# Kernel tuning notes

Hardware: AMD Instinct MI355X
Metric: run time of the kernel (lower is better)

The kernel has to match this reference:

```python
import jax, jax.numpy as jnp
import numpy as np

HEAD = 2

def setup_inputs() -> dict:
    key = jax.random.key(0)
    ks = jax.random.split(key, 12)
    B, C, H, W = 4, 512, 64, 64
    IC = 256
    N = H * W
    s = 0.02
    return {
        "x": jax.random.normal(ks[0], (B, C, H, W), jnp.float32),
        "output_attn": jax.random.normal(ks[1], (B, C, H, W), jnp.float32),
        "mlp_w": jax.random.normal(ks[2], (N, N), jnp.float32) * s,
        "mlp_b": jax.random.normal(ks[3], (N,), jnp.float32) * s,
        "g_w": jax.random.normal(ks[4], (IC, C), jnp.float32) * s,
        "g_b": jax.random.normal(ks[5], (IC,), jnp.float32) * s,
        "theta_w": jax.random.normal(ks[6], (IC, C), jnp.float32) * s,
        "theta_b": jax.random.normal(ks[7], (IC,), jnp.float32) * s,
        "phi_w": jax.random.normal(ks[8], (IC, C), jnp.float32) * s,
        "phi_b": jax.random.normal(ks[9], (IC,), jnp.float32) * s,
        "out_w": jax.random.normal(ks[10], (C, IC), jnp.float32) * s,
        "out_b": jax.random.normal(ks[11], (C,), jnp.float32) * s,
    }

def _conv1x1(feat, w, b):
    # feat: [B, Cin, N], w: [Cout, Cin], b: [Cout] -> [B, Cout, N]
    return jnp.einsum('bcn,oc->bon', feat, w) + b[None, :, None]

def reference(x, output_attn, mlp_w, mlp_b, g_w, g_b, theta_w, theta_b,
              phi_w, phi_b, out_w, out_b):
    B, C, H, W = x.shape
    N = H * W
    IC = g_w.shape[0]
    d = IC // HEAD  # per-head dim

    xf = x.reshape(B, C, N)
    # head-MLP remix: only hd==HEAD slice is non-empty (integer-division bug in source)
    xf = xf + (jnp.einsum('bcn,mn->bcm', xf, mlp_w) + mlp_b)

    g = _conv1x1(xf, g_w, g_b)                       # [B, IC, N]
    g = g.reshape(B * HEAD, d, N).transpose(0, 2, 1)  # [BH, N, d]

    oa = output_attn.reshape(B, C, N)
    th = _conv1x1(oa, theta_w, theta_b).reshape(B * HEAD, d, N).transpose(0, 2, 1)  # [BH, N, d]
    ph = _conv1x1(xf, phi_w, phi_b).reshape(B * HEAD, d, N)                          # [BH, d, N]

    scale = 1.0 / (d ** 0.5)
    attn = jax.nn.softmax(jnp.einsum('bnd,bdm->bnm', th, ph) * scale, axis=-1)  # [BH, N, N]
    y = jnp.einsum('bnm,bmd->bnd', attn, g)           # [BH, N, d]
    y = y.reshape(B, HEAD, N, d).transpose(0, 2, 1, 3).reshape(B, N, IC)
    y = y.transpose(0, 2, 1)                          # [B, IC, N]

    out = output_attn + _conv1x1(y, out_w, out_b).reshape(B, C, H, W)
    return out
```

## Files before the change

### kernel.cpp

```cpp
#include <hip/hip_runtime.h>

typedef unsigned short us;
typedef us s8v __attribute__((ext_vector_type(8)));
typedef us s4v __attribute__((ext_vector_type(4)));
typedef float f4v __attribute__((ext_vector_type(4)));
typedef float f16v __attribute__((ext_vector_type(16)));
typedef __bf16 b2v __attribute__((ext_vector_type(2)));

static __device__ __forceinline__ us f2b(float f) {
  return __builtin_bit_cast(us, (__bf16)f);
}
static __device__ __forceinline__ unsigned f2b2(float lo, float hi) {
  b2v v = {(__bf16)lo, (__bf16)hi};
  return __builtin_bit_cast(unsigned, v);
}
static __device__ __forceinline__ float b2f(us s) {
  unsigned u = ((unsigned)s) << 16;
  return __builtin_bit_cast(float, u);
}

#define GLDS(src, dst)                                                        \
  __builtin_amdgcn_global_load_lds(                                           \
      (const __attribute__((address_space(1))) unsigned int*)(src),           \
      (__attribute__((address_space(3))) unsigned int*)(dst), 16, 0, 0)

__global__ __launch_bounds__(256) void castk(const float* __restrict__ in,
                                             us* __restrict__ out, int n4) {
  int i = blockIdx.x * 256 + threadIdx.x;
  int stride = gridDim.x * 256;
  for (; i < n4; i += stride) {
    float4 v = ((const float4*)in)[i];
    s4v s = {f2b(v.x), f2b(v.y), f2b(v.z), f2b(v.w)};
    ((s4v*)out)[i] = s;
  }
}

__global__ __launch_bounds__(256) void wcast4(const float* __restrict__ s0, us* __restrict__ o0,
                                              const float* __restrict__ s1, us* __restrict__ o1,
                                              const float* __restrict__ s2, us* __restrict__ o2,
                                              const float* __restrict__ s3, us* __restrict__ o3) {
  const float* s; us* o;
  int y = blockIdx.y;
  if (y == 0) { s = s0; o = o0; }
  else if (y == 1) { s = s1; o = o1; }
  else if (y == 2) { s = s2; o = o2; }
  else { s = s3; o = o3; }
  int i = blockIdx.x * 256 + threadIdx.x;
  for (; i < 32768; i += 8192) {
    float4 v = ((const float4*)s)[i];
    s4v r = {f2b(v.x), f2b(v.y), f2b(v.z), f2b(v.w)};
    ((s4v*)o)[i] = r;
  }
}

__global__ __launch_bounds__(256) void tcast(const float* __restrict__ in,
                                             us* __restrict__ out, int R, int C) {
  __shared__ float t[64][65];
  const int tid = threadIdx.x;
  const long r0 = (long)blockIdx.y * 64, c0 = (long)blockIdx.x * 64;
#pragma unroll
  for (int j = 0; j < 4; ++j) {
    int idx = j * 256 + tid;
    int row = idx >> 4, c4 = (idx & 15) * 4;
    float4 v = *(const float4*)(in + (r0 + row) * C + c0 + c4);
    t[row][c4] = v.x; t[row][c4 + 1] = v.y; t[row][c4 + 2] = v.z; t[row][c4 + 3] = v.w;
  }
  __syncthreads();
#pragma unroll
  for (int j = 0; j < 4; ++j) {
    int idx = j * 256 + tid;
    int orow = idx >> 4, r4 = (idx & 15) * 4;
    s4v s = {f2b(t[r4][orow]), f2b(t[r4 + 1][orow]), f2b(t[r4 + 2][orow]), f2b(t[r4 + 3][orow])};
    *(s4v*)(out + (c0 + orow) * R + r0 + r4) = s;
  }
}

#define SW(row, kb) ((row) * 128 + ((kb) ^ (((row) & 7) << 4)))

template <int EPI, int AF32, int BF32, int SWZ>
__global__ __launch_bounds__(256) void gemm_nt(
    const void* __restrict__ Av, const void* __restrict__ Bv,
    int lda, int ldb, int K, long aZ, long bZ,
    const float* __restrict__ bias,
    const us* __restrict__ addb16,
    const float* __restrict__ addf32,
    us* __restrict__ outb16,
    float* __restrict__ outf32) {
  __shared__ __align__(16) us lA[128 * 64];
  __shared__ __align__(16) us lB[128 * 64];
  const int tid = threadIdx.x, l = tid & 63;
  const int lr = l & 15, lg = l >> 4;
  const int w = tid >> 6, wr = w >> 1, wc = w & 1;
  int bm, bn;
  if constexpr (SWZ) {
    int flat = blockIdx.y * gridDim.x + blockIdx.x;
    int re = (flat & 7) * ((gridDim.x * gridDim.y) >> 3) + (flat >> 3);
    bm = re % gridDim.x; bn = re / gridDim.x;
  } else { bm = blockIdx.x; bn = blockIdx.y; }
  const int z = blockIdx.z;
  const f4v zero = {0.f, 0.f, 0.f, 0.f};
  f4v acc[4][4];
#pragma unroll
  for (int i = 0; i < 4; ++i)
#pragma unroll
    for (int j = 0; j < 4; ++j) acc[i][j] = zero;
  char* lab = (char*)lA;
  char* lbb = (char*)lB;

  for (int k0 = 0; k0 < K; k0 += 64) {
#pragma unroll
    for (int j = 0; j < 4; ++j) {
      int byte = j * 4096 + tid * 16;
      int row = byte >> 7, kb = byte & 127;
      if constexpr (AF32) {
        const float* af = (const float*)Av + (long)z * aZ + (long)(bm * 128 + row) * lda + k0 + (kb >> 1);
        float4 v0 = *(const float4*)af, v1 = *(const float4*)(af + 4);
        s8v va = {f2b(v0.x), f2b(v0.y), f2b(v0.z), f2b(v0.w), f2b(v1.x), f2b(v1.y), f2b(v1.z), f2b(v1.w)};
        *(s8v*)(lab + SW(row, kb)) = va;
      } else {
        s8v va = *(const s8v*)((const char*)Av + ((long)z * aZ + (long)(bm * 128 + row) * lda + k0) * 2 + kb);
        *(s8v*)(lab + SW(row, kb)) = va;
      }
      if constexpr (BF32) {
        const float* bf_ = (const float*)Bv + (long)z * bZ + (long)(bn * 128 + row) * ldb + k0 + (kb >> 1);
        float4 v0 = *(const float4*)bf_, v1 = *(const float4*)(bf_ + 4);
        s8v vb = {f2b(v0.x), f2b(v0.y), f2b(v0.z), f2b(v0.w), f2b(v1.x), f2b(v1.y), f2b(v1.z), f2b(v1.w)};
        *(s8v*)(lbb + SW(row, kb)) = vb;
      } else {
        s8v vb = *(const s8v*)((const char*)Bv + ((long)z * bZ + (long)(bn * 128 + row) * ldb + k0) * 2 + kb);
        *(s8v*)(lbb + SW(row, kb)) = vb;
      }
    }
    __syncthreads();
#pragma unroll
    for (int ks = 0; ks < 2; ++ks) {
      s8v af[4], bf[4];
      const int kb = ks * 64 + lg * 16;
#pragma unroll
      for (int mi = 0; mi < 4; ++mi) {
        int row = wr * 64 + mi * 16 + lr;
        af[mi] = *(const s8v*)(lab + SW(row, kb));
      }
#pragma unroll
      for (int ni = 0; ni < 4; ++ni) {
        int row = wc * 64 + ni * 16 + lr;
        bf[ni] = *(const s8v*)(lbb + SW(row, kb));
      }
#pragma unroll
      for (int mi = 0; mi < 4; ++mi)
#pragma unroll
        for (int ni = 0; ni < 4; ++ni)
          acc[mi][ni] = __builtin_amdgcn_mfma_f32_16x16x32_bf16(af[mi], bf[ni], acc[mi][ni], 0, 0, 0);
    }
    __syncthreads();
  }

#pragma unroll
  for (int mi = 0; mi < 4; ++mi) {
#pragma unroll
    for (int ni = 0; ni < 4; ++ni) {
#pragma unroll
      for (int r = 0; r < 4; ++r) {
        int row = bm * 128 + wr * 64 + mi * 16 + lg * 4 + r;
        int col = bn * 128 + wc * 64 + ni * 16 + lr;
        float v = acc[mi][ni][r];
        if constexpr (EPI == 0) {
          long idx = (long)row * 2048 + col;
          outb16[idx] = f2b(v + b2f(addb16[idx]) + bias[row]);
        } else if constexpr (EPI == 1) {
          long idx = ((long)(z * 2 + (col >> 7)) * 4096 + row) * 128 + (col & 127);
          outb16[idx] = f2b(v + bias[col]);
        } else if constexpr (EPI == 2) {
          long idx = ((long)(z * 256 + row)) * 4096 + col;
          outb16[idx] = f2b(v + bias[row]);
        } else {
          long idx = ((long)(z * 512 + row)) * 4096 + col;
          outf32[idx] = v + bias[row] + addf32[idx];
        }
      }
    }
  }
}

__global__ __launch_bounds__(256, 2) void attn_k(const us* __restrict__ th,
                                                 const us* __restrict__ pht,
                                                 const us* __restrict__ g,
                                                 us* __restrict__ pY,
                                                 float2* __restrict__ pml) {
  __shared__ __align__(16) us ph2[2][64 * 128];
  __shared__ __align__(16) us g2[2][128 * 64];
  const int tid = threadIdx.x, l = tid & 63, w = tid >> 6;
  const int l31 = l & 31, h = l >> 5;
  const int swz = (l & 7) << 4;
  const int flat = blockIdx.y * 32 + blockIdx.x;
  const int bh = flat & 7, rest = flat >> 3;
  const int half = rest & 1, qb = rest >> 1;
  const int b = bh >> 1, head = bh & 1;
  const int m00 = half * 2048;
  const float C1 = 0.12751802f;
  const f16v zero16 = {0.f};

  const char* phsrc = (const char*)(pht + (long)bh * 4096 * 128);
  const char* gsrc = (const char*)(g + (long)(b * 256 + head * 128) * 4096);

  int koff[4], voff[4];
#pragma unroll
  for (int j = 0; j < 4; ++j) {
    int d = j * 4096 + tid * 16;
    koff[j] = d ^ (((d >> 8) & 7) << 4);
    int rowg = d >> 7, kbg = d & 127;
    voff[j] = rowg * 8192 + (kbg ^ ((rowg & 7) << 4));
  }

  s8v qf[8];
  {
    const us* thp = th + ((long)bh * 4096 + qb * 128 + w * 32 + l31) * 128 + h * 8;
#pragma unroll
    for (int ks = 0; ks < 8; ++ks) qf[ks] = *(const s8v*)(thp + ks * 16);
  }

  f16v acc0 = zero16, acc1 = zero16, acc2 = zero16, acc3 = zero16;
  float m_run = -1e30f, l_run = 0.f;

  auto stage = [&](int bufi, int m0) {
    char* dk = (char*)ph2[bufi] + w * 1024;
    char* dv = (char*)g2[bufi] + w * 1024;
    const char* sk = phsrc + (long)m0 * 256;
    const char* sv = gsrc + (long)m0 * 2;
#pragma unroll
    for (int j = 0; j < 4; ++j) {
      GLDS(sk + koff[j], dk + j * 4096);
      GLDS(sv + voff[j], dv + j * 4096);
    }
  };

  stage(0, m00);
  __syncthreads();

  for (int t = 0; t < 32; ++t) {
    const int cur = t & 1;
    stage(cur ^ 1, m00 + ((t + 1) & 31) * 64);
    const char* phb = (const char*)ph2[cur];
    const char* gb = (const char*)g2[cur];

    f16v sA[2] = {zero16, zero16};
    __builtin_amdgcn_s_setprio(1);
#pragma unroll
    for (int ks = 0; ks < 8; ++ks) {
      const int kb = (ks * 32) ^ swz;
#pragma unroll
      for (int mt = 0; mt < 2; ++mt) {
        s8v kf = *(const s8v*)(phb + (mt * 32 + l31) * 256 + (((ks * 32) + h * 16) ^ swz));
        sA[mt] = __builtin_amdgcn_mfma_f32_32x32x16_bf16(kf, qf[ks], sA[mt], 0, 0, 0);
      }
      (void)kb;
    }
    __builtin_amdgcn_s_setprio(0);

    float mx = sA[0][0];
#pragma unroll
    for (int r = 1; r < 16; ++r) mx = fmaxf(mx, sA[0][r]);
#pragma unroll
    for (int r = 0; r < 16; ++r) mx = fmaxf(mx, sA[1][r]);
    mx = fmaxf(mx, __shfl_xor(mx, 32, 64));

    if (__any(mx > m_run + 60.0f)) {
      float mn = fmaxf(m_run, mx);
      float corr = __builtin_amdgcn_exp2f((m_run - mn) * C1);
      m_run = mn;
      l_run *= corr;
#pragma unroll
      for (int r = 0; r < 16; ++r) {
        acc0[r] *= corr; acc1[r] *= corr; acc2[r] *= corr; acc3[r] *= corr;
      }
    }

    const float nm = -m_run * C1;
    float sum = 0.f;
    s8v bfrag[4];
#pragma unroll
    for (int mt = 0; mt < 2; ++mt) {
#pragma unroll
      for (int k1 = 0; k1 < 2; ++k1) {
        const int base = k1 * 8;
        float p0 = __builtin_amdgcn_exp2f(__builtin_fmaf(sA[mt][base + 0], C1, nm));
        float p1 = __builtin_amdgcn_exp2f(__builtin_fmaf(sA[mt][base + 1], C1, nm));
        float p2 = __builtin_amdgcn_exp2f(__builtin_fmaf(sA[mt][base + 2], C1, nm));
        float p3 = __builtin_amdgcn_exp2f(__builtin_fmaf(sA[mt][base + 3], C1, nm));
        float p4 = __builtin_amdgcn_exp2f(__builtin_fmaf(sA[mt][base + 4], C1, nm));
        float p5 = __builtin_amdgcn_exp2f(__builtin_fmaf(sA[mt][base + 5], C1, nm));
        float p6 = __builtin_amdgcn_exp2f(__builtin_fmaf(sA[mt][base + 6], C1, nm));
        float p7 = __builtin_amdgcn_exp2f(__builtin_fmaf(sA[mt][base + 7], C1, nm));
        sum += ((p0 + p1) + (p2 + p3)) + ((p4 + p5) + (p6 + p7));
        unsigned E0 = f2b2(p0, p1), E1 = f2b2(p2, p3);
        unsigned O0 = f2b2(p4, p5), O1 = f2b2(p6, p7);
        asm("v_permlane32_swap_b32 %0, %1" : "+v"(E0), "+v"(O0));
        asm("v_permlane32_swap_b32 %0, %1" : "+v"(E1), "+v"(O1));
        uint4 u = {E0, E1, O0, O1};
        bfrag[mt * 2 + k1] = __builtin_bit_cast(s8v, u);
      }
    }
    sum += __shfl_xor(sum, 32, 64);
    l_run += sum;

    __builtin_amdgcn_s_setprio(1);
#pragma unroll
    for (int ks2 = 0; ks2 < 4; ++ks2) {
      const int kb = ((ks2 * 32) + h * 16) ^ swz;
      s8v v0 = *(const s8v*)(gb + (l31) * 128 + kb);
      s8v v1 = *(const s8v*)(gb + (32 + l31) * 128 + kb);
      s8v v2 = *(const s8v*)(gb + (64 + l31) * 128 + kb);
      s8v v3 = *(const s8v*)(gb + (96 + l31) * 128 + kb);
      acc0 = __builtin_amdgcn_mfma_f32_32x32x16_bf16(v0, bfrag[ks2], acc0, 0, 0, 0);
      acc1 = __builtin_amdgcn_mfma_f32_32x32x16_bf16(v1, bfrag[ks2], acc1, 0, 0, 0);
      acc2 = __builtin_amdgcn_mfma_f32_32x32x16_bf16(v2, bfrag[ks2], acc2, 0, 0, 0);
      acc3 = __builtin_amdgcn_mfma_f32_32x32x16_bf16(v3, bfrag[ks2], acc3, 0, 0, 0);
    }
    __builtin_amdgcn_s_setprio(0);

    __syncthreads();
  }

  const long gq = (long)bh * 4096 + qb * 128 + w * 32 + l31;
  if (h == 0) pml[gq * 2 + half] = make_float2(m_run, l_run);
  us* py = pY + (gq * 2 + half) * 128;
#pragma unroll
  for (int gi = 0; gi < 4; ++gi) {
    int r0 = gi * 4;
    {
      uint2 u = {f2b2(acc0[r0], acc0[r0 + 1]), f2b2(acc0[r0 + 2], acc0[r0 + 3])};
      *(uint2*)(py + gi * 8 + 4 * h) = u;
    }
    {
      uint2 u = {f2b2(acc1[r0], acc1[r0 + 1]), f2b2(acc1[r0 + 2], acc1[r0 + 3])};
      *(uint2*)(py + 32 + gi * 8 + 4 * h) = u;
    }
    {
      uint2 u = {f2b2(acc2[r0], acc2[r0 + 1]), f2b2(acc2[r0 + 2], acc2[r0 + 3])};
      *(uint2*)(py + 64 + gi * 8 + 4 * h) = u;
    }
    {
      uint2 u = {f2b2(acc3[r0], acc3[r0 + 1]), f2b2(acc3[r0 + 2], acc3[r0 + 3])};
      *(uint2*)(py + 96 + gi * 8 + 4 * h) = u;
    }
  }
}

__global__ __launch_bounds__(256) void mergek(const us* __restrict__ pY,
                                              const float2* __restrict__ pml,
                                              us* __restrict__ yt) {
  const float C1 = 0.12751802f;
  int idx = blockIdx.x * 256 + threadIdx.x;
  int gq = idx >> 4, dd8 = (idx & 15) * 8;
  float2 A = pml[gq * 2 + 0], B = pml[gq * 2 + 1];
  float M = fmaxf(A.x, B.x);
  float e0 = __builtin_amdgcn_exp2f((A.x - M) * C1);
  float e1 = __builtin_amdgcn_exp2f((B.x - M) * C1);
  float inv = 1.0f / (A.y * e0 + B.y * e1);
  e0 *= inv; e1 *= inv;
  s8v Y0 = *(const s8v*)(pY + ((long)gq * 2 + 0) * 128 + dd8);
  s8v Y1 = *(const s8v*)(pY + ((long)gq * 2 + 1) * 128 + dd8);
  s8v o;
#pragma unroll
  for (int i = 0; i < 8; ++i) o[i] = f2b(e0 * b2f(Y0[i]) + e1 * b2f(Y1[i]));
  int bh = gq >> 12, q = gq & 4095, b = bh >> 1, head = bh & 1;
  *(s8v*)(yt + ((long)b * 4096 + q) * 256 + head * 128 + dd8) = o;
}

extern "C" void kernel_launch(void* const* d_in, const int* in_sizes, int n_in,
                              void* d_out, int out_size, void* d_ws, size_t ws_size,
                              hipStream_t stream) {
  (void)in_sizes; (void)n_in; (void)out_size;
  const float* x       = (const float*)d_in[0];
  const float* oa      = (const float*)d_in[1];
  const float* mlp_w   = (const float*)d_in[2];
  const float* mlp_b   = (const float*)d_in[3];
  const float* g_w     = (const float*)d_in[4];
  const float* g_b     = (const float*)d_in[5];
  const float* theta_w = (const float*)d_in[6];
  const float* theta_b = (const float*)d_in[7];
  const float* phi_w   = (const float*)d_in[8];
  const float* phi_b   = (const float*)d_in[9];
  const float* out_w   = (const float*)d_in[10];
  const float* out_b   = (const float*)d_in[11];
  float* out = (float*)d_out;
  char* ws = (char*)d_ws;

  us* xf_t   = (us*)(ws + 0L);
  us* pY     = (us*)(ws + 0L);
  us* oat    = (us*)(ws + 16777216L);
  float2* pml = (float2*)(ws + 16777216L);
  us* xt     = (us*)(ws + 33554432L);
  us* g_ws   = (us*)(ws + 33554432L);
  us* th_ws  = (us*)(ws + 41943040L);
  us* xc     = (us*)(ws + 50331648L);
  us* ph_ws  = (us*)(ws + 50331648L);
  us* yt     = (us*)(ws + 58720256L);
  us* g_wb   = (us*)(ws + 67108864L);
  us* th_wb  = (us*)(ws + 67371008L);
  us* ph_wb  = (us*)(ws + 67633152L);
  us* out_wb = (us*)(ws + 67895296L);
  us* mlp_wb = (us*)(ws + 68157440L);
  const bool big = ws_size >= 101711872ULL;

  wcast4<<<dim3(32, 4), dim3(256), 0, stream>>>(g_w, g_wb, theta_w, th_wb,
                                                phi_w, ph_wb, out_w, out_wb);
  castk<<<dim3(1024), dim3(256), 0, stream>>>(x, xc, 2097152);
  tcast<<<dim3(64, 32), dim3(256), 0, stream>>>(x, xt, 2048, 4096);
  tcast<<<dim3(64, 32), dim3(256), 0, stream>>>(oa, oat, 2048, 4096);

  if (big) {
    castk<<<dim3(1024), dim3(256), 0, stream>>>(mlp_w, mlp_wb, 4194304);
    gemm_nt<0, 0, 0, 1><<<dim3(32, 16, 1), dim3(256), 0, stream>>>(
        mlp_wb, xc, 4096, 4096, 4096, 0, 0, mlp_b, xt, nullptr, xf_t, nullptr);
  } else {
    gemm_nt<0, 1, 0, 1><<<dim3(32, 16, 1), dim3(256), 0, stream>>>(
        mlp_w, xc, 4096, 4096, 4096, 0, 0, mlp_b, xt, nullptr, xf_t, nullptr);
  }

  gemm_nt<1, 0, 0, 0><<<dim3(32, 2, 4), dim3(256), 0, stream>>>(
      oat, th_wb, 2048, 512, 512, 512, 0, theta_b, nullptr, nullptr, th_ws, nullptr);
  gemm_nt<1, 0, 0, 0><<<dim3(32, 2, 4), dim3(256), 0, stream>>>(
      xf_t, ph_wb, 2048, 512, 512, 512, 0, phi_b, nullptr, nullptr, ph_ws, nullptr);
  gemm_nt<2, 0, 0, 0><<<dim3(2, 32, 4), dim3(256), 0, stream>>>(
      g_wb, xf_t, 512, 2048, 512, 0, 512, g_b, nullptr, nullptr, g_ws, nullptr);

  attn_k<<<dim3(32, 16), dim3(256), 0, stream>>>(th_ws, ph_ws, g_ws, pY, pml);
  mergek<<<dim3(2048), dim3(256), 0, stream>>>(pY, pml, yt);

  gemm_nt<3, 0, 0, 0><<<dim3(4, 32, 4), dim3(256), 0, stream>>>(
      out_wb, yt, 256, 256, 256, 0, 1048576L, out_b, nullptr, oa, nullptr, out);
}
```

Baseline: 280.3 us.

## Use direct global-to-LDS loads in bf16 GEMM and fuse x cast into transpose

For bf16 operands, the GEMM now loads tiles straight from global memory into LDS with global_load_lds and pre-swizzled source addresses, instead of staging them through registers. The next tile's load is issued right after the barrier, which restructures the loop's synchronisation. The separate castk pass over x is folded into the transpose-cast kernel, which now also writes the row-major bf16 copy and saves one read of x. The GEMM is still single-buffered, so load and compute overlap stays limited, and the swizzled addressing must exactly match the MFMA fragment reads.

```diff
diff --git a/kernel.cpp b/kernel.cpp
--- a/kernel.cpp
+++ b/kernel.cpp
@@ -54,7 +54,8 @@
 }
 
 __global__ __launch_bounds__(256) void tcast(const float* __restrict__ in,
-                                             us* __restrict__ out, int R, int C) {
+                                             us* __restrict__ out, int R, int C,
+                                             us* __restrict__ out2) {
   __shared__ float t[64][65];
   const int tid = threadIdx.x;
   const long r0 = (long)blockIdx.y * 64, c0 = (long)blockIdx.x * 64;
@@ -64,6 +65,10 @@
     int row = idx >> 4, c4 = (idx & 15) * 4;
     float4 v = *(const float4*)(in + (r0 + row) * C + c0 + c4);
     t[row][c4] = v.x; t[row][c4 + 1] = v.y; t[row][c4 + 2] = v.z; t[row][c4 + 3] = v.w;
+    if (out2) {
+      s4v s = {f2b(v.x), f2b(v.y), f2b(v.z), f2b(v.w)};
+      *(s4v*)(out2 + (r0 + row) * C + c0 + c4) = s;
+    }
   }
   __syncthreads();
 #pragma unroll
@@ -107,30 +112,44 @@
   char* lab = (char*)lA;
   char* lbb = (char*)lB;
 
-  for (int k0 = 0; k0 < K; k0 += 64) {
+  int rS[4], cS[4];
+#pragma unroll
+  for (int j = 0; j < 4; ++j) {
+    int byte = j * 4096 + tid * 16;
+    rS[j] = byte >> 7;
+    cS[j] = (byte & 127) ^ ((rS[j] & 7) << 4);
+  }
+  const char* Ab = (const char*)Av + ((long)z * aZ + (long)bm * 128 * lda) * 2;
+  const char* Bb = (const char*)Bv + ((long)z * bZ + (long)bn * 128 * ldb) * 2;
+
+  auto stage = [&](int k0) {
 #pragma unroll
     for (int j = 0; j < 4; ++j) {
-      int byte = j * 4096 + tid * 16;
-      int row = byte >> 7, kb = byte & 127;
       if constexpr (AF32) {
+        int byte = j * 4096 + tid * 16;
+        int row = byte >> 7, kb = byte & 127;
         const float* af = (const float*)Av + (long)z * aZ + (long)(bm * 128 + row) * lda + k0 + (kb >> 1);
         float4 v0 = *(const float4*)af, v1 = *(const float4*)(af + 4);
         s8v va = {f2b(v0.x), f2b(v0.y), f2b(v0.z), f2b(v0.w), f2b(v1.x), f2b(v1.y), f2b(v1.z), f2b(v1.w)};
         *(s8v*)(lab + SW(row, kb)) = va;
       } else {
-        s8v va = *(const s8v*)((const char*)Av + ((long)z * aZ + (long)(bm * 128 + row) * lda + k0) * 2 + kb);
-        *(s8v*)(lab + SW(row, kb)) = va;
+        GLDS(Ab + (long)rS[j] * lda * 2 + k0 * 2 + cS[j], lab + j * 4096 + w * 1024);
       }
       if constexpr (BF32) {
+        int byte = j * 4096 + tid * 16;
+        int row = byte >> 7, kb = byte & 127;
         const float* bf_ = (const float*)Bv + (long)z * bZ + (long)(bn * 128 + row) * ldb + k0 + (kb >> 1);
         float4 v0 = *(const float4*)bf_, v1 = *(const float4*)(bf_ + 4);
         s8v vb = {f2b(v0.x), f2b(v0.y), f2b(v0.z), f2b(v0.w), f2b(v1.x), f2b(v1.y), f2b(v1.z), f2b(v1.w)};
         *(s8v*)(lbb + SW(row, kb)) = vb;
       } else {
-        s8v vb = *(const s8v*)((const char*)Bv + ((long)z * bZ + (long)(bn * 128 + row) * ldb + k0) * 2 + kb);
-        *(s8v*)(lbb + SW(row, kb)) = vb;
-      }
-    }
+        GLDS(Bb + (long)rS[j] * ldb * 2 + k0 * 2 + cS[j], lbb + j * 4096 + w * 1024);
+      }
+    }
+  };
+
+  stage(0);
+  for (int k0 = 0; k0 < K; k0 += 64) {
     __syncthreads();
 #pragma unroll
     for (int ks = 0; ks < 2; ++ks) {
@@ -152,7 +171,10 @@
         for (int ni = 0; ni < 4; ++ni)
           acc[mi][ni] = __builtin_amdgcn_mfma_f32_16x16x32_bf16(af[mi], bf[ni], acc[mi][ni], 0, 0, 0);
     }
-    __syncthreads();
+    if (k0 + 64 < K) {
+      __syncthreads();
+      stage(k0 + 64);
+    }
   }
 
 #pragma unroll
@@ -247,13 +269,11 @@
     __builtin_amdgcn_s_setprio(1);
 #pragma unroll
     for (int ks = 0; ks < 8; ++ks) {
-      const int kb = (ks * 32) ^ swz;
 #pragma unroll
       for (int mt = 0; mt < 2; ++mt) {
         s8v kf = *(const s8v*)(phb + (mt * 32 + l31) * 256 + (((ks * 32) + h * 16) ^ swz));
         sA[mt] = __builtin_amdgcn_mfma_f32_32x32x16_bf16(kf, qf[ks], sA[mt], 0, 0, 0);
       }
-      (void)kb;
     }
     __builtin_amdgcn_s_setprio(0);
 
@@ -405,9 +425,8 @@
 
   wcast4<<<dim3(32, 4), dim3(256), 0, stream>>>(g_w, g_wb, theta_w, th_wb,
                                                 phi_w, ph_wb, out_w, out_wb);
-  castk<<<dim3(1024), dim3(256), 0, stream>>>(x, xc, 2097152);
-  tcast<<<dim3(64, 32), dim3(256), 0, stream>>>(x, xt, 2048, 4096);
-  tcast<<<dim3(64, 32), dim3(256), 0, stream>>>(oa, oat, 2048, 4096);
+  tcast<<<dim3(64, 32), dim3(256), 0, stream>>>(x, xt, 2048, 4096, xc);
+  tcast<<<dim3(64, 32), dim3(256), 0, stream>>>(oa, oat, 2048, 4096, nullptr);
 
   if (big) {
     castk<<<dim3(1024), dim3(256), 0, stream>>>(mlp_w, mlp_wb, 4194304);
```

Result: faster. 270.6 us (-3.5%).
